# Optimization experiments

Hardware: AMD Instinct MI355X
Metric: run time of the kernel (lower is better)

Reference implementation:

```python
import jax, jax.numpy as jnp
import numpy as np

DIM = 1024
SCALE = DIM ** (-0.5)
TEMPERATURE = 1.0


def setup_inputs() -> dict:
    key = jax.random.key(0)
    ks = jax.random.split(key, 7)
    B, N, D = 8, 4096, DIM
    s = 1.0 / np.sqrt(D)
    return {
        "x": jax.random.normal(ks[0], (B, N, D), dtype=jnp.float32),
        "Wq": jax.random.normal(ks[1], (D, D), dtype=jnp.float32) * s,
        "bq": jax.random.normal(ks[2], (D,), dtype=jnp.float32) * 0.01,
        "Wk": jax.random.normal(ks[3], (D, D), dtype=jnp.float32) * s,
        "bk": jax.random.normal(ks[4], (D,), dtype=jnp.float32) * 0.01,
        "Wv": jax.random.normal(ks[5], (D, D), dtype=jnp.float32) * s,
        "bv": jax.random.normal(ks[6], (D,), dtype=jnp.float32) * 0.01,
    }


def reference(x, Wq, bq, Wk, bk, Wv, bv):
    B, N, D = x.shape
    # adaptive_avg_pool1d from N -> N//2 with N even == mean over adjacent pairs
    q_input = x.reshape(B, N // 2, 2, D).mean(axis=2)  # [B, N/2, D]
    # torch Linear: y = x @ W.T + b
    q = jnp.einsum("bmd,ed->bme", q_input, Wq) + bq      # [B, N/2, D]
    k = jnp.einsum("bnd,ed->bne", x, Wk) + bk            # [B, N, D]
    v = jnp.einsum("bnd,ed->bne", x, Wv) + bv            # [B, N, D]
    attn = jnp.einsum("bmd,bnd->bmn", q, k) * SCALE      # [B, N/2, N]
    attn = jax.nn.softmax(attn * TEMPERATURE, axis=-1)
    k_out = jnp.einsum("bmn,bnd->bmd", attn, v)          # [B, N/2, D]
    return (q, k_out, k_out)
```

## Files before the change

### kernel.cpp

```cpp
#include <hip/hip_runtime.h>
#include <hip/hip_bf16.h>
#include <cstddef>

typedef __attribute__((ext_vector_type(8))) short s16x8;
typedef __attribute__((ext_vector_type(4))) short s16x4;
typedef __attribute__((ext_vector_type(4))) float f32x4;

#define MFMA_BF16(a, b, c) __builtin_amdgcn_mfma_f32_16x16x32_bf16((a), (b), (c), 0, 0, 0)

__device__ __forceinline__ short f2bf(float f) {
    union { float f; unsigned u; } cv; cv.f = f;
    unsigned u = cv.u;
    unsigned r = (u + 0x7FFFu + ((u >> 16) & 1u)) >> 16;
    return (short)r;
}
__device__ __forceinline__ float bf2f(unsigned short u) {
    union { unsigned u; float f; } cv; cv.u = ((unsigned)u) << 16; return cv.f;
}

__device__ __forceinline__ void gl16(const void* g, void* l) {
    __builtin_amdgcn_global_load_lds(
        (const __attribute__((address_space(1))) void*)g,
        (__attribute__((address_space(3))) void*)l, 16, 0, 0);
}

template <int MODE>
__global__ __launch_bounds__(256, 2) void gemm_bf(
    const void* __restrict__ Ap, const short* __restrict__ Bp,
    const float* __restrict__ bias, const float* __restrict__ lvec,
    void* __restrict__ Cp, void* __restrict__ Cp2)
{
    constexpr int NT  = (MODE == 4) ? 64 : 16;
    constexpr int LDA = (MODE == 4) ? 4096 : 1024;
    constexpr int LDB = (MODE == 4) ? 4096 : 1024;

    __shared__ short As[128 * 64];
    __shared__ short Bs[128 * 64];
    const int tid = threadIdx.x;

    int bx, by, z;
    if constexpr (MODE == 1 || MODE == 3 || MODE == 4 || MODE == 5) {
        const int n = blockIdx.x;
        constexpr int NBY = (MODE == 1) ? 8 : 16;
        z = n & 7; const int m = n >> 3; by = m % NBY; bx = m / NBY;
    } else { bx = blockIdx.x; by = blockIdx.y; z = blockIdx.z; }

    const int w = tid >> 6, l = tid & 63, l15 = l & 15, lhi = l >> 4;
    const int wy = w >> 1, wx = w & 1;
    const int X = (l15 & 7) << 3;
    const int lr8 = l >> 3, cb = l & 7, scb = cb ^ lr8;

    size_t arow0 = (size_t)by * 128, brow0 = (size_t)bx * 128;
    if constexpr (MODE == 3 || MODE == 4 || MODE == 5) arow0 += (size_t)z * 2048;
    if constexpr (MODE == 1 || MODE == 3 || MODE == 5) brow0 += (size_t)z * 4096;
    if constexpr (MODE == 4) brow0 += (size_t)z * 1024;

    const short* Ab = (const short*)Ap;
    const float* Af = (const float*)Ap;

    const short* gA = Ab + (arow0 + w * 32 + lr8) * (size_t)LDA + scb * 8;
    const short* gB = Bp + (brow0 + w * 32 + lr8) * (size_t)LDB + scb * 8;

    f32x4 acc[4][4];
    #pragma unroll
    for (int m = 0; m < 4; ++m)
        #pragma unroll
        for (int n = 0; n < 4; ++n) acc[m][n] = (f32x4){0.f, 0.f, 0.f, 0.f};

    const int r0b = tid >> 3, cb8 = (tid & 7) * 8;
    const int r0f = tid >> 4, kcs = tid & 15;

    for (int kt = 0; kt < NT; ++kt) {
        #pragma unroll
        for (int i = 0; i < 4; ++i)
            gl16(gB + (size_t)(i * 8) * LDB + kt * 64, &Bs[(w * 32 + i * 8) * 64]);
        if constexpr (MODE == 2) {
            #pragma unroll
            for (int p = 0; p < 4; ++p) {
                const int r = r0b + p * 32;
                const size_t g = (arow0 + r) * 2048 + kt * 64 + cb8;
                s16x8 u0 = *(const s16x8*)(Ab + g);
                s16x8 u1 = *(const s16x8*)(Ab + g + 1024);
                s16x8 o;
                #pragma unroll
                for (int j = 0; j < 8; ++j)
                    o[j] = f2bf(0.5f * (bf2f((unsigned short)u0[j]) + bf2f((unsigned short)u1[j])));
                *(s16x8*)&As[r * 64 + (cb8 ^ ((r & 7) * 8))] = o;
            }
        } else if constexpr (MODE == 3) {
            const int k0 = kt * 64 + kcs * 4;
            #pragma unroll
            for (int p = 0; p < 8; ++p) {
                const int r = r0f + p * 16;
                float4 u = *(const float4*)(Af + (arow0 + r) * 1024 + k0);
                s16x4 sa = { f2bf(u.x * 0.03125f), f2bf(u.y * 0.03125f),
                             f2bf(u.z * 0.03125f), f2bf(u.w * 0.03125f) };
                *(s16x4*)&As[r * 64 + ((kcs * 4) ^ ((r & 7) * 8))] = sa;
            }
        } else {
            #pragma unroll
            for (int i = 0; i < 4; ++i)
                gl16(gA + (size_t)(i * 8) * LDA + kt * 64, &As[(w * 32 + i * 8) * 64]);
        }
        __syncthreads();
        #pragma unroll
        for (int kk = 0; kk < 2; ++kk) {
            const int e = (kk * 32 + lhi * 8) ^ X;
            s16x8 af[4], bfr[4];
            #pragma unroll
            for (int m = 0; m < 4; ++m)
                af[m] = *(const s16x8*)&As[(wy * 64 + m * 16 + l15) * 64 + e];
            #pragma unroll
            for (int n = 0; n < 4; ++n)
                bfr[n] = *(const s16x8*)&Bs[(wx * 64 + n * 16 + l15) * 64 + e];
            #pragma unroll
            for (int m = 0; m < 4; ++m)
                #pragma unroll
                for (int n = 0; n < 4; ++n)
                    acc[m][n] = MFMA_BF16(af[m], bfr[n], acc[m][n]);
        }
        __syncthreads();
    }

    #pragma unroll
    for (int m = 0; m < 4; ++m) {
        #pragma unroll
        for (int j = 0; j < 4; ++j) {
            const int rl = wy * 64 + m * 16 + lhi * 4 + j;
            const int grow = by * 128 + rl;
            float radd = 0.f, rmul = 1.f;
            if constexpr (MODE == 1) radd = bias[grow];
            if constexpr (MODE == 4) rmul = 1.0f / lvec[(size_t)z * 2048 + grow];
            #pragma unroll
            for (int n = 0; n < 4; ++n) {
                const int cl = wx * 64 + n * 16 + l15;
                const int gcol = bx * 128 + cl;
                float v = acc[m][n][j];
                if constexpr (MODE == 0) {
                    ((short*)Cp)[(size_t)grow * 1024 + gcol] = f2bf(v + bias[gcol]);
                } else if constexpr (MODE == 1) {
                    ((short*)Cp)[(size_t)z * 4194304 + (size_t)grow * 4096 + gcol] = f2bf(v + radd);
                } else if constexpr (MODE == 2) {
                    const float qv = v + bias[gcol];
                    ((float*)Cp)[(size_t)grow * 1024 + gcol] = qv;
                    if (Cp2 != nullptr)
                        ((short*)Cp2)[(size_t)grow * 1024 + gcol] = f2bf(qv * 0.03125f);
                } else if constexpr (MODE == 3 || MODE == 5) {
                    ((short*)Cp)[(size_t)z * 8388608 + (size_t)grow * 4096 + gcol] = f2bf(v);
                } else {
                    const size_t o = ((size_t)z * 2048 + grow) * 1024 + gcol;
                    const float ov = v * rmul;
                    ((float*)Cp)[o] = ov;
                    ((float*)Cp2)[o] = ov;
                }
            }
        }
    }
}

template <int MODE>
__global__ __launch_bounds__(256, 2) void gemm_f32(
    const float* __restrict__ Ap, const float* __restrict__ Bp,
    const float* __restrict__ bias, void* __restrict__ Cp, void* __restrict__ Cp2)
{
    constexpr int LDA = (MODE == 2) ? 2048 : 1024;
    __shared__ short As[128 * 64];
    __shared__ short Bs[128 * 64];
    const int tid = threadIdx.x;
    const int bx = blockIdx.x, by = blockIdx.y, z = blockIdx.z;
    const int w = tid >> 6, l = tid & 63, l15 = l & 15, lhi = l >> 4;
    const int wy = w >> 1, wx = w & 1;
    const int X = (l15 & 7) << 3;

    size_t arow0 = (size_t)by * 128, brow0 = (size_t)bx * 128;
    if constexpr (MODE == 1) brow0 += (size_t)z * 4096;

    f32x4 acc[4][4];
    #pragma unroll
    for (int m = 0; m < 4; ++m)
        #pragma unroll
        for (int n = 0; n < 4; ++n) acc[m][n] = (f32x4){0.f, 0.f, 0.f, 0.f};

    const int r0f = tid >> 4, kcs = tid & 15;
    float4 ra[8], ra2[8], rb[8];

    auto load_tile = [&](int kt) {
        const int k0 = kt * 64 + kcs * 4;
        #pragma unroll
        for (int p = 0; p < 8; ++p) {
            const int r = r0f + p * 16;
            if constexpr (MODE == 2) {
                const float* s0 = Ap + (arow0 + r) * (size_t)LDA + k0;
                ra[p] = *(const float4*)s0;
                ra2[p] = *(const float4*)(s0 + 1024);
            } else {
                ra[p] = *(const float4*)(Ap + (arow0 + r) * (size_t)LDA + k0);
            }
            rb[p] = *(const float4*)(Bp + (brow0 + r) * (size_t)1024 + k0);
        }
    };

    load_tile(0);
    for (int kt = 0; kt < 16; ++kt) {
        #pragma unroll
        for (int p = 0; p < 8; ++p) {
            const int r = r0f + p * 16;
            const int e = (kcs * 4) ^ ((r & 7) << 3);
            float ax, ay, az, aw;
            if constexpr (MODE == 2) {
                ax = 0.5f * (ra[p].x + ra2[p].x); ay = 0.5f * (ra[p].y + ra2[p].y);
                az = 0.5f * (ra[p].z + ra2[p].z); aw = 0.5f * (ra[p].w + ra2[p].w);
            } else {
                ax = ra[p].x; ay = ra[p].y; az = ra[p].z; aw = ra[p].w;
            }
            s16x4 sa = { f2bf(ax), f2bf(ay), f2bf(az), f2bf(aw) };
            *(s16x4*)&As[r * 64 + e] = sa;
            s16x4 sb = { f2bf(rb[p].x), f2bf(rb[p].y), f2bf(rb[p].z), f2bf(rb[p].w) };
            *(s16x4*)&Bs[r * 64 + e] = sb;
        }
        if (kt + 1 < 16) load_tile(kt + 1);
        __syncthreads();
        #pragma unroll
        for (int kk = 0; kk < 2; ++kk) {
            const int e = (kk * 32 + lhi * 8) ^ X;
            s16x8 af[4], bfr[4];
            #pragma unroll
            for (int m = 0; m < 4; ++m)
                af[m] = *(const s16x8*)&As[(wy * 64 + m * 16 + l15) * 64 + e];
            #pragma unroll
            for (int n = 0; n < 4; ++n)
                bfr[n] = *(const s16x8*)&Bs[(wx * 64 + n * 16 + l15) * 64 + e];
            #pragma unroll
            for (int m = 0; m < 4; ++m)
                #pragma unroll
                for (int n = 0; n < 4; ++n)
                    acc[m][n] = MFMA_BF16(af[m], bfr[n], acc[m][n]);
        }
        __syncthreads();
    }

    #pragma unroll
    for (int m = 0; m < 4; ++m) {
        #pragma unroll
        for (int j = 0; j < 4; ++j) {
            const int rl = wy * 64 + m * 16 + lhi * 4 + j;
            const int grow = by * 128 + rl;
            const float radd = (MODE == 1) ? bias[grow] : 0.f;
            #pragma unroll
            for (int n = 0; n < 4; ++n) {
                const int cl = wx * 64 + n * 16 + l15;
                const int gcol = bx * 128 + cl;
                float v = acc[m][n][j];
                if constexpr (MODE == 0) {
                    ((short*)Cp)[(size_t)grow * 1024 + gcol] = f2bf(v + bias[gcol]);
                } else if constexpr (MODE == 1) {
                    ((short*)Cp)[(size_t)z * 4194304 + (size_t)grow * 4096 + gcol] = f2bf(v + radd);
                } else {
                    const float q = v + bias[gcol];
                    ((float*)Cp)[(size_t)grow * 1024 + gcol] = q;
                    ((short*)Cp2)[(size_t)grow * 1024 + gcol] = f2bf(q * 0.03125f);
                }
            }
        }
    }
}

__global__ __launch_bounds__(256, 4) void convert_x(const float* __restrict__ x,
                                                    short* __restrict__ xb)
{
    const size_t i0 = ((size_t)blockIdx.x * 256 + threadIdx.x) * 8;
    float4 a = *(const float4*)(x + i0), b = *(const float4*)(x + i0 + 4);
    s16x8 o = { f2bf(a.x), f2bf(a.y), f2bf(a.z), f2bf(a.w),
                f2bf(b.x), f2bf(b.y), f2bf(b.z), f2bf(b.w) };
    *(s16x8*)(xb + i0) = o;
}

__global__ __launch_bounds__(256, 4) void convert_w(
    const float* __restrict__ Wq, const float* __restrict__ Wk,
    const float* __restrict__ Wv, short* __restrict__ Wb)
{
    const int gid = blockIdx.x * 256 + threadIdx.x;
    const int seg = gid >> 17;
    const size_t off = (size_t)(gid & 131071) * 8;
    const float* s = (seg == 0) ? Wq : ((seg == 1) ? Wk : Wv);
    float4 a = *(const float4*)(s + off), b = *(const float4*)(s + off + 4);
    s16x8 o = { f2bf(a.x), f2bf(a.y), f2bf(a.z), f2bf(a.w),
                f2bf(b.x), f2bf(b.y), f2bf(b.z), f2bf(b.w) };
    *(s16x8*)(Wb + (size_t)seg * 1048576 + off) = o;
}

__global__ __launch_bounds__(256, 4) void softmax_rows(
    const unsigned short* __restrict__ Sin, unsigned short* __restrict__ Pout,
    float* __restrict__ lvec)
{
    const int w = threadIdx.x >> 6, l = threadIdx.x & 63;
    const int row = blockIdx.x * 4 + w;
    const unsigned short* rp = Sin + (size_t)row * 4096;
    unsigned short* wp = Pout + (size_t)row * 4096;

    s16x8 v[8];
    #pragma unroll
    for (int c = 0; c < 8; ++c)
        v[c] = *(const s16x8*)(rp + (c * 64 + l) * 8);

    float mx = -1e30f;
    #pragma unroll
    for (int c = 0; c < 8; ++c)
        #pragma unroll
        for (int j = 0; j < 8; ++j)
            mx = fmaxf(mx, bf2f((unsigned short)v[c][j]));
    #pragma unroll
    for (int d = 1; d < 64; d <<= 1) mx = fmaxf(mx, __shfl_xor(mx, d));

    float sum = 0.f;
    #pragma unroll
    for (int c = 0; c < 8; ++c) {
        #pragma unroll
        for (int j = 0; j < 8; ++j) {
            const float p = __expf(bf2f((unsigned short)v[c][j]) - mx);
            sum += p;
            v[c][j] = f2bf(p);
        }
    }
    #pragma unroll
    for (int d = 1; d < 64; d <<= 1) sum += __shfl_xor(sum, d);

    #pragma unroll
    for (int c = 0; c < 8; ++c)
        *(s16x8*)(wp + (c * 64 + l) * 8) = v[c];
    if (l == 0) lvec[row] = sum;
}

__global__ __launch_bounds__(256, 4) void dup_out(
    const float4* __restrict__ O, float4* __restrict__ o1, float4* __restrict__ o2)
{
    const size_t i0 = (size_t)blockIdx.x * 256 + threadIdx.x;
    #pragma unroll
    for (int p = 0; p < 4; ++p) {
        const size_t i = i0 + (size_t)p * 1048576;
        const float4 t = O[i];
        o1[i] = t;
        o2[i] = t;
    }
}

extern "C" void kernel_launch(void* const* d_in, const int* in_sizes, int n_in,
                              void* d_out, int out_size, void* d_ws, size_t ws_size,
                              hipStream_t stream) {
    const float* x  = (const float*)d_in[0];
    const float* Wq = (const float*)d_in[1];
    const float* bq = (const float*)d_in[2];
    const float* Wk = (const float*)d_in[3];
    const float* bk = (const float*)d_in[4];
    const float* Wv = (const float*)d_in[5];
    const float* bv = (const float*)d_in[6];

    float* out   = (float*)d_out;
    float* q_out = out;
    float* out1  = out + (size_t)16777216;
    float* out2  = out + (size_t)33554432;
    short* Smat  = (short*)out1;

    const unsigned long long NEED_A2 = 241434624ULL;
    const unsigned long long NEED_A1 = 207683584ULL;

    if ((unsigned long long)ws_size >= NEED_A2) {
        short* xb  = (short*)d_ws;
        short* Wb  = xb + (size_t)33554432;
        short* kws = Wb + (size_t)3145728;
        short* vT  = kws + (size_t)33554432;
        short* qs  = vT + (size_t)33554432;
        float* lws = (float*)(qs + (size_t)16777216);
        unsigned short* Pws = (unsigned short*)d_ws;

        convert_x<<<dim3(16384, 1, 1), 256, 0, stream>>>(x, xb);
        convert_w<<<dim3(1536, 1, 1), 256, 0, stream>>>(Wq, Wk, Wv, Wb);
        gemm_bf<0><<<dim3(8, 256, 1), 256, 0, stream>>>(xb, Wb + 1048576, bk, nullptr, (void*)kws, nullptr);
        gemm_bf<1><<<dim3(2048, 1, 1), 256, 0, stream>>>(Wb + 2097152, xb, bv, nullptr, (void*)vT, nullptr);
        gemm_bf<2><<<dim3(8, 128, 1), 256, 0, stream>>>(xb, Wb, bq, nullptr, (void*)q_out, (void*)qs);
        gemm_bf<5><<<dim3(4096, 1, 1), 256, 0, stream>>>(qs, kws, nullptr, nullptr, (void*)Smat, nullptr);
        softmax_rows<<<dim3(4096, 1, 1), 256, 0, stream>>>((const unsigned short*)Smat, Pws, lws);
        gemm_bf<4><<<dim3(1024, 1, 1), 256, 0, stream>>>(Pws, vT, nullptr, lws, (void*)out1, (void*)out2);
    } else if ((unsigned long long)ws_size >= NEED_A1) {
        short* xb  = (short*)d_ws;
        short* Wb  = xb + (size_t)33554432;
        short* kws = Wb + (size_t)3145728;
        short* vT  = kws + (size_t)33554432;
        float* lws = (float*)((char*)d_ws + 207618048ULL);
        unsigned short* Pws = (unsigned short*)d_ws;

        convert_x<<<dim3(16384, 1, 1), 256, 0, stream>>>(x, xb);
        convert_w<<<dim3(1536, 1, 1), 256, 0, stream>>>(Wq, Wk, Wv, Wb);
        gemm_bf<0><<<dim3(8, 256, 1), 256, 0, stream>>>(xb, Wb + 1048576, bk, nullptr, (void*)kws, nullptr);
        gemm_bf<1><<<dim3(2048, 1, 1), 256, 0, stream>>>(Wb + 2097152, xb, bv, nullptr, (void*)vT, nullptr);
        gemm_bf<2><<<dim3(8, 128, 1), 256, 0, stream>>>(xb, Wb, bq, nullptr, (void*)q_out, nullptr);
        gemm_bf<3><<<dim3(4096, 1, 1), 256, 0, stream>>>(q_out, kws, nullptr, nullptr, (void*)Smat, nullptr);
        softmax_rows<<<dim3(4096, 1, 1), 256, 0, stream>>>((const unsigned short*)Smat, Pws, lws);
        gemm_bf<4><<<dim3(1024, 1, 1), 256, 0, stream>>>(Pws, vT, nullptr, lws, (void*)out1, (void*)out2);
    } else {
        short* kws = (short*)d_ws;
        short* vT  = kws + (size_t)33554432;
        short* qs  = vT + (size_t)33554432;
        float* lws = (float*)((char*)d_ws + 167772160ULL);
        float* Ows = (float*)d_ws;

        gemm_f32<0><<<dim3(8, 256, 1), 256, 0, stream>>>(x, Wk, bk, (void*)kws, nullptr);
        gemm_f32<1><<<dim3(32, 8, 8), 256, 0, stream>>>(Wv, x, bv, (void*)vT, nullptr);
        gemm_f32<2><<<dim3(8, 128, 1), 256, 0, stream>>>(x, Wq, bq, (void*)q_out, (void*)qs);
        gemm_bf<5><<<dim3(4096, 1, 1), 256, 0, stream>>>(qs, kws, nullptr, nullptr, (void*)Smat, nullptr);
        softmax_rows<<<dim3(4096, 1, 1), 256, 0, stream>>>((const unsigned short*)Smat, (unsigned short*)Smat, lws);
        gemm_bf<4><<<dim3(1024, 1, 1), 256, 0, stream>>>(Smat, vT, nullptr, lws, (void*)Ows, (void*)Ows);
        dup_out<<<dim3(4096, 1, 1), 256, 0, stream>>>((const float4*)Ows, (float4*)out1, (float4*)out2);
    }
}
```

Baseline: 652.8 us.

## Fuse exp into QK^T GEMM epilogue, drop softmax pass, process batches in halves

The QK^T GEMM epilogue now writes exp(scores) as bf16 directly and stores per-tile partial row sums, so the separate softmax kernel goes away. A small reduce kernel sums the partials into the normalizer, which the PV GEMM applies. Batches run in two halves of four so the P buffer fits in the workspace alongside the partial sums. The risk is that exponentiating without subtracting the row max can overflow for large scores, and the extra launches add overhead.

```diff
diff --git a/kernel.cpp b/kernel.cpp
--- a/kernel.cpp
+++ b/kernel.cpp
@@ -28,18 +28,22 @@
 __global__ __launch_bounds__(256, 2) void gemm_bf(
     const void* __restrict__ Ap, const short* __restrict__ Bp,
     const float* __restrict__ bias, const float* __restrict__ lvec,
-    void* __restrict__ Cp, void* __restrict__ Cp2)
-{
-    constexpr int NT  = (MODE == 4) ? 64 : 16;
-    constexpr int LDA = (MODE == 4) ? 4096 : 1024;
-    constexpr int LDB = (MODE == 4) ? 4096 : 1024;
+    void* __restrict__ Cp, void* __restrict__ Cp2,
+    int zbase, float* __restrict__ lpart)
+{
+    constexpr int NT  = (MODE == 4 || MODE == 7) ? 64 : 16;
+    constexpr int LDA = (MODE == 4 || MODE == 7) ? 4096 : 1024;
+    constexpr int LDB = (MODE == 4 || MODE == 7) ? 4096 : 1024;
 
     __shared__ short As[128 * 64];
     __shared__ short Bs[128 * 64];
     const int tid = threadIdx.x;
 
     int bx, by, z;
-    if constexpr (MODE == 1 || MODE == 3 || MODE == 4 || MODE == 5) {
+    if constexpr (MODE == 6 || MODE == 7) {
+        const int n = blockIdx.x;
+        z = (n & 3) + zbase; const int m = n >> 2; by = m % 16; bx = m / 16;
+    } else if constexpr (MODE == 1 || MODE == 3 || MODE == 4 || MODE == 5) {
         const int n = blockIdx.x;
         constexpr int NBY = (MODE == 1) ? 8 : 16;
         z = n & 7; const int m = n >> 3; by = m % NBY; bx = m / NBY;
@@ -51,9 +55,10 @@
     const int lr8 = l >> 3, cb = l & 7, scb = cb ^ lr8;
 
     size_t arow0 = (size_t)by * 128, brow0 = (size_t)bx * 128;
-    if constexpr (MODE == 3 || MODE == 4 || MODE == 5) arow0 += (size_t)z * 2048;
-    if constexpr (MODE == 1 || MODE == 3 || MODE == 5) brow0 += (size_t)z * 4096;
-    if constexpr (MODE == 4) brow0 += (size_t)z * 1024;
+    if constexpr (MODE == 3 || MODE == 4 || MODE == 5 || MODE == 6) arow0 += (size_t)z * 2048;
+    if constexpr (MODE == 7) arow0 += (size_t)(z & 3) * 2048;
+    if constexpr (MODE == 1 || MODE == 3 || MODE == 5 || MODE == 6) brow0 += (size_t)z * 4096;
+    if constexpr (MODE == 4 || MODE == 7) brow0 += (size_t)z * 1024;
 
     const short* Ab = (const short*)Ap;
     const float* Af = (const float*)Ap;
@@ -130,32 +135,60 @@
             const int grow = by * 128 + rl;
             float radd = 0.f, rmul = 1.f;
             if constexpr (MODE == 1) radd = bias[grow];
-            if constexpr (MODE == 4) rmul = 1.0f / lvec[(size_t)z * 2048 + grow];
-            #pragma unroll
-            for (int n = 0; n < 4; ++n) {
-                const int cl = wx * 64 + n * 16 + l15;
-                const int gcol = bx * 128 + cl;
-                float v = acc[m][n][j];
-                if constexpr (MODE == 0) {
-                    ((short*)Cp)[(size_t)grow * 1024 + gcol] = f2bf(v + bias[gcol]);
-                } else if constexpr (MODE == 1) {
-                    ((short*)Cp)[(size_t)z * 4194304 + (size_t)grow * 4096 + gcol] = f2bf(v + radd);
-                } else if constexpr (MODE == 2) {
-                    const float qv = v + bias[gcol];
-                    ((float*)Cp)[(size_t)grow * 1024 + gcol] = qv;
-                    if (Cp2 != nullptr)
-                        ((short*)Cp2)[(size_t)grow * 1024 + gcol] = f2bf(qv * 0.03125f);
-                } else if constexpr (MODE == 3 || MODE == 5) {
-                    ((short*)Cp)[(size_t)z * 8388608 + (size_t)grow * 4096 + gcol] = f2bf(v);
-                } else {
-                    const size_t o = ((size_t)z * 2048 + grow) * 1024 + gcol;
-                    const float ov = v * rmul;
-                    ((float*)Cp)[o] = ov;
-                    ((float*)Cp2)[o] = ov;
+            if constexpr (MODE == 4 || MODE == 7) rmul = 1.0f / lvec[(size_t)z * 2048 + grow];
+            if constexpr (MODE == 6) {
+                float s = 0.f;
+                #pragma unroll
+                for (int n = 0; n < 4; ++n) {
+                    const int gcol = bx * 128 + wx * 64 + n * 16 + l15;
+                    const float pv = __expf(acc[m][n][j]);
+                    s += pv;
+                    ((short*)Cp)[(size_t)(z & 3) * 8388608 + (size_t)grow * 4096 + gcol] = f2bf(pv);
                 }
-            }
-        }
-    }
+                s += __shfl_xor(s, 1);
+                s += __shfl_xor(s, 2);
+                s += __shfl_xor(s, 4);
+                s += __shfl_xor(s, 8);
+                if (l15 == 0)
+                    lpart[((size_t)(z & 3) * 2048 + grow) * 64 + bx * 2 + wx] = s;
+            } else {
+                #pragma unroll
+                for (int n = 0; n < 4; ++n) {
+                    const int cl = wx * 64 + n * 16 + l15;
+                    const int gcol = bx * 128 + cl;
+                    float v = acc[m][n][j];
+                    if constexpr (MODE == 0) {
+                        ((short*)Cp)[(size_t)grow * 1024 + gcol] = f2bf(v + bias[gcol]);
+                    } else if constexpr (MODE == 1) {
+                        ((short*)Cp)[(size_t)z * 4194304 + (size_t)grow * 4096 + gcol] = f2bf(v + radd);
+                    } else if constexpr (MODE == 2) {
+                        const float qv = v + bias[gcol];
+                        ((float*)Cp)[(size_t)grow * 1024 + gcol] = qv;
+                        if (Cp2 != nullptr)
+                            ((short*)Cp2)[(size_t)grow * 1024 + gcol] = f2bf(qv * 0.03125f);
+                    } else if constexpr (MODE == 3 || MODE == 5) {
+                        ((short*)Cp)[(size_t)z * 8388608 + (size_t)grow * 4096 + gcol] = f2bf(v);
+                    } else {
+                        const size_t o = ((size_t)z * 2048 + grow) * 1024 + gcol;
+                        const float ov = v * rmul;
+                        ((float*)Cp)[o] = ov;
+                        ((float*)Cp2)[o] = ov;
+                    }
+                }
+            }
+        }
+    }
+}
+
+__global__ __launch_bounds__(256, 4) void reduce_l(
+    const float* __restrict__ lpart, float* __restrict__ lvec, int zbase)
+{
+    const int r = blockIdx.x * 256 + threadIdx.x;
+    const float4* p = (const float4*)(lpart + (size_t)r * 64);
+    float s = 0.f;
+    #pragma unroll
+    for (int i = 0; i < 16; ++i) { float4 v = p[i]; s += v.x + v.y + v.z + v.w; }
+    lvec[(size_t)zbase * 2048 + r] = s;
 }
 
 template <int MODE>
@@ -371,16 +404,20 @@
         short* vT  = kws + (size_t)33554432;
         short* qs  = vT + (size_t)33554432;
         float* lws = (float*)(qs + (size_t)16777216);
-        unsigned short* Pws = (unsigned short*)d_ws;
+        short* Pws   = (short*)d_ws;
+        float* lpart = (float*)((char*)d_ws + 67108864);
 
         convert_x<<<dim3(16384, 1, 1), 256, 0, stream>>>(x, xb);
         convert_w<<<dim3(1536, 1, 1), 256, 0, stream>>>(Wq, Wk, Wv, Wb);
-        gemm_bf<0><<<dim3(8, 256, 1), 256, 0, stream>>>(xb, Wb + 1048576, bk, nullptr, (void*)kws, nullptr);
-        gemm_bf<1><<<dim3(2048, 1, 1), 256, 0, stream>>>(Wb + 2097152, xb, bv, nullptr, (void*)vT, nullptr);
-        gemm_bf<2><<<dim3(8, 128, 1), 256, 0, stream>>>(xb, Wb, bq, nullptr, (void*)q_out, (void*)qs);
-        gemm_bf<5><<<dim3(4096, 1, 1), 256, 0, stream>>>(qs, kws, nullptr, nullptr, (void*)Smat, nullptr);
-        softmax_rows<<<dim3(4096, 1, 1), 256, 0, stream>>>((const unsigned short*)Smat, Pws, lws);
-        gemm_bf<4><<<dim3(1024, 1, 1), 256, 0, stream>>>(Pws, vT, nullptr, lws, (void*)out1, (void*)out2);
+        gemm_bf<0><<<dim3(8, 256, 1), 256, 0, stream>>>(xb, Wb + 1048576, bk, nullptr, (void*)kws, nullptr, 0, nullptr);
+        gemm_bf<1><<<dim3(2048, 1, 1), 256, 0, stream>>>(Wb + 2097152, xb, bv, nullptr, (void*)vT, nullptr, 0, nullptr);
+        gemm_bf<2><<<dim3(8, 128, 1), 256, 0, stream>>>(xb, Wb, bq, nullptr, (void*)q_out, (void*)qs, 0, nullptr);
+        for (int half = 0; half < 2; ++half) {
+            const int zb = half * 4;
+            gemm_bf<6><<<dim3(2048, 1, 1), 256, 0, stream>>>(qs, kws, nullptr, nullptr, (void*)Pws, nullptr, zb, lpart);
+            reduce_l<<<dim3(32, 1, 1), 256, 0, stream>>>(lpart, lws, zb);
+            gemm_bf<7><<<dim3(512, 1, 1), 256, 0, stream>>>(Pws, vT, nullptr, lws, (void*)out1, (void*)out2, zb, nullptr);
+        }
     } else if ((unsigned long long)ws_size >= NEED_A1) {
         short* xb  = (short*)d_ws;
         short* Wb  = xb + (size_t)33554432;
@@ -391,12 +428,12 @@
 
         convert_x<<<dim3(16384, 1, 1), 256, 0, stream>>>(x, xb);
         convert_w<<<dim3(1536, 1, 1), 256, 0, stream>>>(Wq, Wk, Wv, Wb);
-        gemm_bf<0><<<dim3(8, 256, 1), 256, 0, stream>>>(xb, Wb + 1048576, bk, nullptr, (void*)kws, nullptr);
-        gemm_bf<1><<<dim3(2048, 1, 1), 256, 0, stream>>>(Wb + 2097152, xb, bv, nullptr, (void*)vT, nullptr);
-        gemm_bf<2><<<dim3(8, 128, 1), 256, 0, stream>>>(xb, Wb, bq, nullptr, (void*)q_out, nullptr);
-        gemm_bf<3><<<dim3(4096, 1, 1), 256, 0, stream>>>(q_out, kws, nullptr, nullptr, (void*)Smat, nullptr);
+        gemm_bf<0><<<dim3(8, 256, 1), 256, 0, stream>>>(xb, Wb + 1048576, bk, nullptr, (void*)kws, nullptr, 0, nullptr);
+        gemm_bf<1><<<dim3(2048, 1, 1), 256, 0, stream>>>(Wb + 2097152, xb, bv, nullptr, (void*)vT, nullptr, 0, nullptr);
+        gemm_bf<2><<<dim3(8, 128, 1), 256, 0, stream>>>(xb, Wb, bq, nullptr, (void*)q_out, nullptr, 0, nullptr);
+        gemm_bf<3><<<dim3(4096, 1, 1), 256, 0, stream>>>(q_out, kws, nullptr, nullptr, (void*)Smat, nullptr, 0, nullptr);
         softmax_rows<<<dim3(4096, 1, 1), 256, 0, stream>>>((const unsigned short*)Smat, Pws, lws);
-        gemm_bf<4><<<dim3(1024, 1, 1), 256, 0, stream>>>(Pws, vT, nullptr, lws, (void*)out1, (void*)out2);
+        gemm_bf<4><<<dim3(1024, 1, 1), 256, 0, stream>>>(Pws, vT, nullptr, lws, (void*)out1, (void*)out2, 0, nullptr);
     } else {
         short* kws = (short*)d_ws;
         short* vT  = kws + (size_t)33554432;
@@ -407,9 +444,9 @@
         gemm_f32<0><<<dim3(8, 256, 1), 256, 0, stream>>>(x, Wk, bk, (void*)kws, nullptr);
         gemm_f32<1><<<dim3(32, 8, 8), 256, 0, stream>>>(Wv, x, bv, (void*)vT, nullptr);
         gemm_f32<2><<<dim3(8, 128, 1), 256, 0, stream>>>(x, Wq, bq, (void*)q_out, (void*)qs);
-        gemm_bf<5><<<dim3(4096, 1, 1), 256, 0, stream>>>(qs, kws, nullptr, nullptr, (void*)Smat, nullptr);
+        gemm_bf<5><<<dim3(4096, 1, 1), 256, 0, stream>>>(qs, kws, nullptr, nullptr, (void*)Smat, nullptr, 0, nullptr);
         softmax_rows<<<dim3(4096, 1, 1), 256, 0, stream>>>((const unsigned short*)Smat, (unsigned short*)Smat, lws);
-        gemm_bf<4><<<dim3(1024, 1, 1), 256, 0, stream>>>(Smat, vT, nullptr, lws, (void*)Ows, (void*)Ows);
+        gemm_bf<4><<<dim3(1024, 1, 1), 256, 0, stream>>>(Smat, vT, nullptr, lws, (void*)Ows, (void*)Ows, 0, nullptr);
         dup_out<<<dim3(4096, 1, 1), 256, 0, stream>>>((const float4*)Ows, (float4*)out1, (float4*)out2);
     }
 }
```

After: 636.9 us. -2.4%, faster.
